# Performance work log

Measured on AMD Instinct MI355X. Metric: run time of the kernel, lower is better.

Reference implementation:

```python
import jax, jax.numpy as jnp
import numpy as np

N, E, F_NODE, F_EDGE, H, C = 25000, 50000, 7, 2, 4, 512
HC = H * C  # 2048


def setup_inputs() -> dict:
    key = jax.random.key(0)
    ks = jax.random.split(key, 20)
    p = lambda k, shp: (jax.random.normal(k, shp, dtype=jnp.float32) * 0.02)
    return {
        "x": jax.random.normal(ks[0], (N, F_NODE), dtype=jnp.float32),
        "edge_attr": jax.random.normal(ks[1], (E, F_EDGE), dtype=jnp.float32),
        "edge_index": jax.random.randint(ks[2], (2, E), 0, N, dtype=jnp.int64),
        "W_node": p(ks[3], (F_NODE, C)), "b_node": jnp.zeros((C,), jnp.float32),
        "W_edge": p(ks[4], (F_EDGE, C)), "b_edge": jnp.zeros((C,), jnp.float32),
        "W_l": p(ks[5], (C, HC)), "b_l": jnp.zeros((HC,), jnp.float32),
        "W_r": p(ks[6], (C, HC)), "b_r": jnp.zeros((HC,), jnp.float32),
        "W_le": p(ks[7], (C, HC)),  # lin_edge has no bias in PyG GATv2Conv
        "att": p(ks[8], (H, C)),
        "conv_bias": jnp.zeros((HC,), jnp.float32),
        "W_d1": p(ks[9], (HC, C)), "b_d1": jnp.zeros((C,), jnp.float32),
        "W_d2": p(ks[10], (C, 6)), "b_d2": jnp.zeros((6,), jnp.float32),
    }


def reference(x, edge_attr, edge_index, W_node, b_node, W_edge, b_edge,
              W_l, b_l, W_r, b_r, W_le, att, conv_bias, W_d1, b_d1, W_d2, b_d2):
    n = x.shape[0]
    src, dst = edge_index[0], edge_index[1]
    # encoders
    h = jax.nn.relu(x @ W_node + b_node)                  # [N, C]
    ea = jax.nn.relu(edge_attr @ W_edge + b_edge)         # [E, C]
    # GATv2Conv (heads=4, concat, edge_dim, add_self_loops=False)
    xl = (h @ W_l + b_l).reshape(n, H, C)                 # source transform
    xr = (h @ W_r + b_r).reshape(n, H, C)                 # target transform
    ee = (ea @ W_le).reshape(-1, H, C)                    # [E, H, C]
    m = xl[src] + xr[dst] + ee                            # [E, H, C]
    s = jax.nn.leaky_relu(m, negative_slope=0.2)
    logits = jnp.einsum('ehc,hc->eh', s, att)             # [E, H]
    # segment softmax over destination nodes
    mx = jax.ops.segment_max(logits, dst, num_segments=n)
    ex = jnp.exp(logits - mx[dst])
    den = jax.ops.segment_sum(ex, dst, num_segments=n)
    alpha = ex / (den[dst] + 1e-16)                       # [E, H]
    out = jax.ops.segment_sum(alpha[..., None] * xl[src], dst, num_segments=n)
    out = out.reshape(n, HC) + conv_bias                  # [N, 2048]
    # decoder + sigmoid (mode != 'train')
    pred = jax.nn.relu(out @ W_d1 + b_d1) @ W_d2 + b_d2   # [N, 6]
    return jax.nn.sigmoid(pred)
```

## Files before the change

kernel.cpp:

```cpp
#include <hip/hip_runtime.h>
#include <hip/hip_bf16.h>

typedef __attribute__((ext_vector_type(8))) short short8;
typedef __attribute__((ext_vector_type(4))) float f32x4;
typedef unsigned int uint32;

#define GLD16(g, l) __builtin_amdgcn_global_load_lds( \
    (const __attribute__((address_space(1))) unsigned int*)(g), \
    (__attribute__((address_space(3))) unsigned int*)(l), 16, 0, 0)

__device__ __forceinline__ float bfu(unsigned short u) {
    union { uint32 v; float f; } x; x.v = ((uint32)u) << 16; return x.f;
}
__device__ __forceinline__ void storev(float* p, float v) { *p = v; }
__device__ __forceinline__ void storev(__hip_bfloat16* p, float v) { *p = __float2bfloat16(v); }

__global__ __launch_bounds__(256) void transpose_bf16(
    const float* __restrict__ W, __hip_bfloat16* __restrict__ WT, int K, int N)
{
    __shared__ float tile[32][33];
    int k0 = blockIdx.x * 32, n0 = blockIdx.y * 32;
    int tx = threadIdx.x & 31, ty = threadIdx.x >> 5;
    #pragma unroll
    for (int i = 0; i < 32; i += 8)
        tile[ty + i][tx] = W[(size_t)(k0 + ty + i) * N + n0 + tx];
    __syncthreads();
    #pragma unroll
    for (int i = 0; i < 32; i += 8)
        WT[(size_t)(n0 + ty + i) * K + k0 + tx] = __float2bfloat16(tile[tx][ty + i]);
}

__global__ __launch_bounds__(256) void encode_nodes(
    const float* __restrict__ x, const float* __restrict__ Wn,
    const float* __restrict__ bn, __hip_bfloat16* __restrict__ h, int Nn)
{
    int idx = blockIdx.x * 256 + threadIdx.x;
    if (idx >= Nn * 512) return;
    int n = idx >> 9, c = idx & 511;
    float acc = bn[c];
    #pragma unroll
    for (int f = 0; f < 7; ++f) acc += x[n * 7 + f] * Wn[f * 512 + c];
    h[idx] = __float2bfloat16(fmaxf(acc, 0.f));
}

__global__ __launch_bounds__(256) void encode_edges(
    const float* __restrict__ eat, const float* __restrict__ We,
    const float* __restrict__ be, __hip_bfloat16* __restrict__ ea, int E)
{
    int idx = blockIdx.x * 256 + threadIdx.x;
    if (idx >= E * 512) return;
    int e = idx >> 9, c = idx & 511;
    float v = fmaf(eat[e * 2], We[c], fmaf(eat[e * 2 + 1], We[512 + c], be[c]));
    ea[idx] = __float2bfloat16(fmaxf(v, 0.f));
}

template <typename OutT, bool HAS_BIAS>
__global__ __launch_bounds__(256) void mfma_gemm(
    const __hip_bfloat16* __restrict__ A, int lda, long az,
    const __hip_bfloat16* __restrict__ BT, int ldb, long bz,
    const float* __restrict__ bias,
    OutT* __restrict__ C, int ldc, long cz, int M, int K)
{
    __shared__ uint4 As4[512];
    __shared__ uint4 Bs4[512];
    A  += (long)blockIdx.z * az;
    BT += (long)blockIdx.z * bz;
    C  += (long)blockIdx.z * cz;
    const int t = threadIdx.x, lane = t & 63, w = t >> 6;
    const int wr = (w >> 1) * 64, wc = (w & 1) * 64;
    const int col0 = blockIdx.x * 128, row0 = blockIdx.y * 128;
    const int lr = lane & 15, lg = lane >> 4;
    const int r0 = w * 16 + (lane >> 2);
    const int ksw = ((lane & 3) ^ ((lane >> 3) & 3)) * 8;
    const int rsw = (lg ^ ((lr >> 1) & 3)) << 4;

    const __hip_bfloat16* Ap0 = A + (size_t)(row0 + r0) * lda + ksw;
    const __hip_bfloat16* Ap1 = A + (size_t)(row0 + r0 + 64) * lda + ksw;
    const __hip_bfloat16* Bp0 = BT + (size_t)(col0 + r0) * ldb + ksw;
    const __hip_bfloat16* Bp1 = BT + (size_t)(col0 + r0 + 64) * ldb + ksw;
    char* AsB = (char*)As4; char* BsB = (char*)Bs4;
    uint4* la0 = As4 + w * 64;       uint4* la1 = As4 + (w + 4) * 64;
    uint4* lb0 = Bs4 + w * 64;       uint4* lb1 = Bs4 + (w + 4) * 64;

    f32x4 acc[4][4];
    #pragma unroll
    for (int m = 0; m < 4; ++m)
        #pragma unroll
        for (int n = 0; n < 4; ++n) acc[m][n] = 0.f;

    for (int k0 = 0; k0 < K; k0 += 32) {
        GLD16(Ap0 + k0, la0);
        GLD16(Ap1 + k0, la1);
        GLD16(Bp0 + k0, lb0);
        GLD16(Bp1 + k0, lb1);
        __syncthreads();
        short8 af[4], bfrag[4];
        #pragma unroll
        for (int m = 0; m < 4; ++m)
            af[m] = *(const short8*)(AsB + (wr + m * 16 + lr) * 64 + rsw);
        #pragma unroll
        for (int n = 0; n < 4; ++n)
            bfrag[n] = *(const short8*)(BsB + (wc + n * 16 + lr) * 64 + rsw);
        #pragma unroll
        for (int m = 0; m < 4; ++m)
            #pragma unroll
            for (int n = 0; n < 4; ++n)
                acc[m][n] = __builtin_amdgcn_mfma_f32_16x16x32_bf16(af[m], bfrag[n], acc[m][n], 0, 0, 0);
        __syncthreads();
    }

    #pragma unroll
    for (int m = 0; m < 4; ++m) {
        #pragma unroll
        for (int r = 0; r < 4; ++r) {
            int gr = row0 + wr + m * 16 + lg * 4 + r;
            if (gr >= M) continue;
            #pragma unroll
            for (int n = 0; n < 4; ++n) {
                int gc = col0 + wc + n * 16 + lr;
                float v = acc[m][n][r];
                if (HAS_BIAS) v += bias[gc];
                storev(&C[(size_t)gr * ldc + gc], v);
            }
        }
    }
}

__global__ __launch_bounds__(256) void edge_mfma_logits(
    const __hip_bfloat16* __restrict__ ea,
    const __hip_bfloat16* __restrict__ WleT,
    const __hip_bfloat16* __restrict__ XL,
    const __hip_bfloat16* __restrict__ XR,
    const int* __restrict__ ei,
    const float* __restrict__ att,
    float* __restrict__ logits,
    int E)
{
    __shared__ uint4 As4[512];
    __shared__ uint4 Bs4[512];
    __shared__ int srcs[128], dsts[128];
    const int t = threadIdx.x, lane = t & 63, w = t >> 6;
    const int wr = (w >> 1) * 64, wc = (w & 1) * 64;
    const int col0 = blockIdx.x * 128, row0 = blockIdx.y * 128;
    const int lr = lane & 15, lg = lane >> 4;
    const int r0 = w * 16 + (lane >> 2);
    const int ksw = ((lane & 3) ^ ((lane >> 3) & 3)) * 8;
    const int rsw = (lg ^ ((lr >> 1) & 3)) << 4;

    if (t < 128) {
        int ge = row0 + t;
        bool ok = ge < E;
        srcs[t] = ok ? ei[ge] : 0;
        dsts[t] = ok ? ei[E + ge] : 0;
    }
    char* AsB = (char*)As4; char* BsB = (char*)Bs4;
    uint4* la0 = As4 + w * 64;       uint4* la1 = As4 + (w + 4) * 64;
    uint4* lb0 = Bs4 + w * 64;       uint4* lb1 = Bs4 + (w + 4) * 64;
    const __hip_bfloat16* Ap0 = ea + (size_t)(row0 + r0) * 512 + ksw;
    const __hip_bfloat16* Ap1 = ea + (size_t)(row0 + r0 + 64) * 512 + ksw;
    const __hip_bfloat16* Bp0 = WleT + (size_t)(col0 + r0) * 512 + ksw;
    const __hip_bfloat16* Bp1 = WleT + (size_t)(col0 + r0 + 64) * 512 + ksw;
    __syncthreads();

    f32x4 acc[4][4];
    #pragma unroll
    for (int m = 0; m < 4; ++m)
        #pragma unroll
        for (int n = 0; n < 4; ++n) acc[m][n] = 0.f;

    for (int k0 = 0; k0 < 512; k0 += 32) {
        GLD16(Ap0 + k0, la0);
        GLD16(Ap1 + k0, la1);
        GLD16(Bp0 + k0, lb0);
        GLD16(Bp1 + k0, lb1);
        __syncthreads();
        short8 af[4], bfrag[4];
        #pragma unroll
        for (int m = 0; m < 4; ++m)
            af[m] = *(const short8*)(AsB + (wr + m * 16 + lr) * 64 + rsw);
        #pragma unroll
        for (int n = 0; n < 4; ++n)
            bfrag[n] = *(const short8*)(BsB + (wc + n * 16 + lr) * 64 + rsw);
        #pragma unroll
        for (int m = 0; m < 4; ++m)
            #pragma unroll
            for (int n = 0; n < 4; ++n)
                acc[m][n] = __builtin_amdgcn_mfma_f32_16x16x32_bf16(af[m], bfrag[n], acc[m][n], 0, 0, 0);
        __syncthreads();
    }

    const int hh = col0 >> 9;
    float attv[4];
    #pragma unroll
    for (int n = 0; n < 4; ++n)
        attv[n] = att[hh * 512 + ((col0 + wc + n * 16 + lr) & 511)];
    float part[4][4];
    #pragma unroll
    for (int m = 0; m < 4; ++m)
        #pragma unroll
        for (int r = 0; r < 4; ++r) part[m][r] = 0.f;

    const int prt = (lane & 3) * 8;
    #pragma unroll
    for (int ch = 0; ch < 4; ++ch) {
        __syncthreads();
        int cc = col0 + ch * 32;
        GLD16(XL + (size_t)srcs[r0] * 2048 + cc + prt, la0);
        GLD16(XL + (size_t)srcs[r0 + 64] * 2048 + cc + prt, la1);
        GLD16(XR + (size_t)dsts[r0] * 2048 + cc + prt, lb0);
        GLD16(XR + (size_t)dsts[r0 + 64] * 2048 + cc + prt, lb1);
        __syncthreads();
        #pragma unroll
        for (int n = 0; n < 4; ++n) {
            if (((wc + n * 16) >> 5) != ch) continue;
            int colin = ((n & 1) << 4) + lr;
            #pragma unroll
            for (int m = 0; m < 4; ++m) {
                #pragma unroll
                for (int r = 0; r < 4; ++r) {
                    int row = wr + m * 16 + lg * 4 + r;
                    float xl = bfu(*(const unsigned short*)(AsB + row * 64 + colin * 2));
                    float xr = bfu(*(const unsigned short*)(BsB + row * 64 + colin * 2));
                    float mv = acc[m][n][r] + xl + xr;
                    part[m][r] += attv[n] * ((mv > 0.f) ? mv : 0.2f * mv);
                }
            }
        }
    }
    #pragma unroll
    for (int m = 0; m < 4; ++m) {
        #pragma unroll
        for (int r = 0; r < 4; ++r) {
            float p = part[m][r];
            p += __shfl_xor(p, 1); p += __shfl_xor(p, 2);
            p += __shfl_xor(p, 4); p += __shfl_xor(p, 8);
            int ge = row0 + wr + m * 16 + lg * 4 + r;
            if (lr == 0 && ge < E) atomicAdd(&logits[ge * 4 + hh], p);
        }
    }
}

__global__ __launch_bounds__(256) void count_dst(
    const int* __restrict__ ei, int* __restrict__ cnt, int E)
{
    int e = blockIdx.x * 256 + threadIdx.x;
    if (e < E) atomicAdd(&cnt[ei[E + e]], 1);
}

__global__ __launch_bounds__(1024) void scan_kernel(
    const int* __restrict__ cnt, int* __restrict__ offs, int N)
{
    __shared__ int wsum[16];
    __shared__ int stot;
    __shared__ int carry_s;
    int t = threadIdx.x, lane = t & 63, w = t >> 6;
    if (t == 0) carry_s = 0;
    __syncthreads();
    for (int base = 0; base < N; base += 1024) {
        int v = (base + t < N) ? cnt[base + t] : 0;
        int x = v;
        #pragma unroll
        for (int off = 1; off < 64; off <<= 1) {
            int y = __shfl_up(x, off);
            if (lane >= off) x += y;
        }
        if (lane == 63) wsum[w] = x;
        __syncthreads();
        if (w == 0 && lane < 16) {
            int v0 = wsum[lane];
            int s = v0;
            #pragma unroll
            for (int off = 1; off < 16; off <<= 1) {
                int y = __shfl_up(s, off);
                if (lane >= off) s += y;
            }
            wsum[lane] = s - v0;
            if (lane == 15) stot = s;
        }
        __syncthreads();
        if (base + t < N) offs[base + t] = carry_s + wsum[w] + x - v;
        __syncthreads();
        if (t == 0) carry_s += stot;
    }
    __syncthreads();
    if (t == 0) offs[N] = carry_s;
}

__global__ __launch_bounds__(256) void fill_elist(
    const int* __restrict__ ei, const int* __restrict__ offs,
    int* __restrict__ cnt2, int* __restrict__ elist, int E)
{
    int e = blockIdx.x * 256 + threadIdx.x;
    if (e >= E) return;
    int d = ei[E + e];
    int p = offs[d] + atomicAdd(&cnt2[d], 1);
    elist[p] = e;
}

__global__ __launch_bounds__(256) void gat_out(
    const __hip_bfloat16* __restrict__ Y,
    const int* __restrict__ ei,
    const int* __restrict__ elist, const int* __restrict__ offs,
    const float* __restrict__ logits,
    const float* __restrict__ bias2,
    const float* __restrict__ Wd2,
    const float* __restrict__ bd2,
    float* __restrict__ out, int N, int E)
{
    __shared__ float wds[512 * 6];
    int t = threadIdx.x;
    for (int i = t; i < 512 * 6; i += 256) wds[i] = Wd2[i];
    __syncthreads();
    int w = t >> 6, lane = t & 63;
    int dst = blockIdx.x * 4 + w;
    if (dst >= N) return;
    int s = offs[dst], cntE = offs[dst + 1] - s;

    float den[4] = {0.f, 0.f, 0.f, 0.f};
    for (int i = 0; i < cntE; ++i) {
        int e = elist[s + i];
        #pragma unroll
        for (int h = 0; h < 4; ++h) den[h] += expf(logits[e * 4 + h]);
    }
    float acc[8] = {0.f, 0.f, 0.f, 0.f, 0.f, 0.f, 0.f, 0.f};
    for (int i = 0; i < cntE; ++i) {
        int e = elist[s + i];
        int src = ei[e];
        #pragma unroll
        for (int h = 0; h < 4; ++h) {
            float al = expf(logits[e * 4 + h]) / (den[h] + 1e-16f);
            uint4 q = *(const uint4*)((const unsigned short*)Y
                        + ((size_t)src * 4 + h) * 512 + lane * 8);
            acc[0] += al * bfu((unsigned short)(q.x & 0xffff));
            acc[1] += al * bfu((unsigned short)(q.x >> 16));
            acc[2] += al * bfu((unsigned short)(q.y & 0xffff));
            acc[3] += al * bfu((unsigned short)(q.y >> 16));
            acc[4] += al * bfu((unsigned short)(q.z & 0xffff));
            acc[5] += al * bfu((unsigned short)(q.z >> 16));
            acc[6] += al * bfu((unsigned short)(q.w & 0xffff));
            acc[7] += al * bfu((unsigned short)(q.w >> 16));
        }
    }
    float p[6] = {0.f, 0.f, 0.f, 0.f, 0.f, 0.f};
    #pragma unroll
    for (int j = 0; j < 8; ++j) {
        int c = lane * 8 + j;
        float u = fmaxf(acc[j] + bias2[c], 0.f);
        #pragma unroll
        for (int jj = 0; jj < 6; ++jj) p[jj] += u * wds[c * 6 + jj];
    }
    #pragma unroll
    for (int off = 32; off; off >>= 1)
        #pragma unroll
        for (int jj = 0; jj < 6; ++jj) p[jj] += __shfl_down(p[jj], off);
    if (lane == 0) {
        #pragma unroll
        for (int jj = 0; jj < 6; ++jj)
            out[(size_t)dst * 6 + jj] = 1.f / (1.f + expf(-(p[jj] + bd2[jj])));
    }
}

__global__ __launch_bounds__(256) void bias2_kernel(
    const float* __restrict__ bd1, const float* __restrict__ cb,
    const float* __restrict__ Wd1, float* __restrict__ bias2)
{
    int j = blockIdx.x * 256 + threadIdx.x;
    if (j >= 512) return;
    float acc = bd1[j];
    for (int k = 0; k < 2048; ++k) acc += cb[k] * Wd1[(size_t)k * 512 + j];
    bias2[j] = acc;
}

extern "C" void kernel_launch(void* const* d_in, const int* in_sizes, int n_in,
                              void* d_out, int out_size, void* d_ws, size_t ws_size,
                              hipStream_t stream)
{
    const float* x         = (const float*)d_in[0];
    const float* edge_attr = (const float*)d_in[1];
    const int*   ei        = (const int*)d_in[2];
    const float* W_node = (const float*)d_in[3],  *b_node = (const float*)d_in[4];
    const float* W_edge = (const float*)d_in[5],  *b_edge = (const float*)d_in[6];
    const float* W_l    = (const float*)d_in[7],  *b_l    = (const float*)d_in[8];
    const float* W_r    = (const float*)d_in[9],  *b_r    = (const float*)d_in[10];
    const float* W_le   = (const float*)d_in[11];
    const float* att    = (const float*)d_in[12];
    const float* conv_bias = (const float*)d_in[13];
    const float* W_d1   = (const float*)d_in[14], *b_d1 = (const float*)d_in[15];
    const float* W_d2   = (const float*)d_in[16], *b_d2 = (const float*)d_in[17];
    float* out = (float*)d_out;

    const int N = in_sizes[0] / 7;
    const int E = in_sizes[1] / 2;
    const int MP = (N + 127) & ~127;
    const int EP = (E + 127) & ~127;

    char* ws = (char*)d_ws;
    const size_t szR0 = (size_t)EP * 512 * 2;
    const size_t szX  = (size_t)MP * 2048 * 2;
    const size_t szW  = (size_t)2048 * 512 * 2;
    const size_t szlg = (size_t)E * 4 * 4;
    const size_t szI  = (((size_t)(N + 1) * 4) + 15) & ~(size_t)15;
    const size_t o_XL = szR0;
    const size_t o_XR = o_XL + szX;
    const size_t o_W  = o_XR + szX;
    const size_t o_lg = o_W + 4 * szW;
    const size_t o_b2 = o_lg + szlg;
    const size_t o_cnt = o_b2 + 2048;
    const size_t o_cnt2 = o_cnt + szI;
    const size_t o_off = o_cnt2 + szI;
    const size_t o_el = o_off + szI;
    const size_t need = o_el + (size_t)E * 4;
    if (ws_size < need) return;

    __hip_bfloat16* h   = (__hip_bfloat16*)ws;
    __hip_bfloat16* ea  = (__hip_bfloat16*)ws;
    __hip_bfloat16* XL  = (__hip_bfloat16*)(ws + o_XL);
    __hip_bfloat16* XR  = (__hip_bfloat16*)(ws + o_XR);
    __hip_bfloat16* Y   = XR;
    __hip_bfloat16* WlT = (__hip_bfloat16*)(ws + o_W);
    __hip_bfloat16* WrT = WlT + szW / 2;
    __hip_bfloat16* WleT= WrT + szW / 2;
    __hip_bfloat16* Wd1T= WleT + szW / 2;
    float* logits = (float*)(ws + o_lg);
    float* bias2  = (float*)(ws + o_b2);
    int* cnt   = (int*)(ws + o_cnt);
    int* cnt2  = (int*)(ws + o_cnt2);
    int* offs  = (int*)(ws + o_off);
    int* elist = (int*)(ws + o_el);

    hipMemsetAsync(logits, 0, szlg, stream);
    hipMemsetAsync(cnt, 0, szI, stream);
    hipMemsetAsync(cnt2, 0, szI, stream);

    dim3 gT(512 / 32, 2048 / 32);
    transpose_bf16<<<gT, 256, 0, stream>>>(W_l,  WlT, 512, 2048);
    transpose_bf16<<<gT, 256, 0, stream>>>(W_r,  WrT, 512, 2048);
    transpose_bf16<<<gT, 256, 0, stream>>>(W_le, WleT, 512, 2048);
    dim3 gT2(2048 / 32, 512 / 32);
    transpose_bf16<<<gT2, 256, 0, stream>>>(W_d1, Wd1T, 2048, 512);
    bias2_kernel<<<2, 256, 0, stream>>>(b_d1, conv_bias, W_d1, bias2);

    count_dst<<<(E + 255) / 256, 256, 0, stream>>>(ei, cnt, E);
    scan_kernel<<<1, 1024, 0, stream>>>(cnt, offs, N);
    fill_elist<<<(E + 255) / 256, 256, 0, stream>>>(ei, offs, cnt2, elist, E);

    encode_nodes<<<(N * 512 + 255) / 256, 256, 0, stream>>>(x, W_node, b_node, h, N);

    const int MB = MP / 128;
    dim3 gNode(2048 / 128, MB);
    mfma_gemm<__hip_bfloat16, true><<<gNode, 256, 0, stream>>>(
        h, 512, 0, WlT, 512, 0, b_l, XL, 2048, 0, N, 512);
    mfma_gemm<__hip_bfloat16, true><<<gNode, 256, 0, stream>>>(
        h, 512, 0, WrT, 512, 0, b_r, XR, 2048, 0, N, 512);

    encode_edges<<<(E * 512 + 255) / 256, 256, 0, stream>>>(edge_attr, W_edge, b_edge, ea, E);

    dim3 gE(16, EP / 128);
    edge_mfma_logits<<<gE, 256, 0, stream>>>(ea, WleT, XL, XR, ei, att, logits, E);

    dim3 gY(512 / 128, MB, 4);
    mfma_gemm<__hip_bfloat16, false><<<gY, 256, 0, stream>>>(
        XL, 2048, 512, Wd1T, 2048, 512, nullptr, Y, 2048, 512, N, 512);

    gat_out<<<(N + 3) / 4, 256, 0, stream>>>(Y, ei, elist, offs, logits,
                                             bias2, W_d2, b_d2, out, N, E);
}
```

Measured before the change: 784.8 us.

## Double-buffer LDS tiles with vmcnt-gated barriers in GEMM and edge-logit kernels

Turns the single-buffered K loop in the MFMA GEMM and the edge logits kernel into a double-buffered pipeline. The next tile's global-to-LDS loads are issued before computing on the current tile, and explicit s_waitcnt vmcnt barriers replace the two __syncthreads per iteration. The gathered XL/XR chunks in the epilogue are prefetched the same way, and the MFMA section runs at raised wave priority. This doubles LDS use per block, which may lower occupancy, and relies on hand-counted vmcnt values being correct.

```diff
diff --git a/kernel.cpp b/kernel.cpp
--- a/kernel.cpp
+++ b/kernel.cpp
@@ -8,6 +8,10 @@
 #define GLD16(g, l) __builtin_amdgcn_global_load_lds( \
     (const __attribute__((address_space(1))) unsigned int*)(g), \
     (__attribute__((address_space(3))) unsigned int*)(l), 16, 0, 0)
+
+#define BAR_VM4()  asm volatile("s_waitcnt vmcnt(4)\ns_barrier" ::: "memory")
+#define BAR_VM0()  asm volatile("s_waitcnt vmcnt(0)\ns_barrier" ::: "memory")
+#define BAR_LGKM() asm volatile("s_waitcnt lgkmcnt(0)\ns_barrier" ::: "memory")
 
 __device__ __forceinline__ float bfu(unsigned short u) {
     union { uint32 v; float f; } x; x.v = ((uint32)u) << 16; return x.f;
@@ -61,8 +65,8 @@
     const float* __restrict__ bias,
     OutT* __restrict__ C, int ldc, long cz, int M, int K)
 {
-    __shared__ uint4 As4[512];
-    __shared__ uint4 Bs4[512];
+    __shared__ uint4 As4[1024];
+    __shared__ uint4 Bs4[1024];
     A  += (long)blockIdx.z * az;
     BT += (long)blockIdx.z * bz;
     C  += (long)blockIdx.z * cz;
@@ -78,9 +82,6 @@
     const __hip_bfloat16* Ap1 = A + (size_t)(row0 + r0 + 64) * lda + ksw;
     const __hip_bfloat16* Bp0 = BT + (size_t)(col0 + r0) * ldb + ksw;
     const __hip_bfloat16* Bp1 = BT + (size_t)(col0 + r0 + 64) * ldb + ksw;
-    char* AsB = (char*)As4; char* BsB = (char*)Bs4;
-    uint4* la0 = As4 + w * 64;       uint4* la1 = As4 + (w + 4) * 64;
-    uint4* lb0 = Bs4 + w * 64;       uint4* lb1 = Bs4 + (w + 4) * 64;
 
     f32x4 acc[4][4];
     #pragma unroll
@@ -88,12 +89,27 @@
         #pragma unroll
         for (int n = 0; n < 4; ++n) acc[m][n] = 0.f;
 
-    for (int k0 = 0; k0 < K; k0 += 32) {
-        GLD16(Ap0 + k0, la0);
-        GLD16(Ap1 + k0, la1);
-        GLD16(Bp0 + k0, lb0);
-        GLD16(Bp1 + k0, lb1);
-        __syncthreads();
+    GLD16(Ap0, As4 + w * 64);
+    GLD16(Ap1, As4 + (w + 4) * 64);
+    GLD16(Bp0, Bs4 + w * 64);
+    GLD16(Bp1, Bs4 + (w + 4) * 64);
+
+    int cur = 0;
+    for (int k0 = 0; k0 < K; k0 += 32, cur ^= 1) {
+        int nk = k0 + 32;
+        if (nk < K) {
+            uint4* a = As4 + (cur ^ 1) * 512;
+            uint4* b = Bs4 + (cur ^ 1) * 512;
+            GLD16(Ap0 + nk, a + w * 64);
+            GLD16(Ap1 + nk, a + (w + 4) * 64);
+            GLD16(Bp0 + nk, b + w * 64);
+            GLD16(Bp1 + nk, b + (w + 4) * 64);
+            BAR_VM4();
+        } else {
+            BAR_VM0();
+        }
+        const char* AsB = (const char*)(As4 + cur * 512);
+        const char* BsB = (const char*)(Bs4 + cur * 512);
         short8 af[4], bfrag[4];
         #pragma unroll
         for (int m = 0; m < 4; ++m)
@@ -101,12 +117,14 @@
         #pragma unroll
         for (int n = 0; n < 4; ++n)
             bfrag[n] = *(const short8*)(BsB + (wc + n * 16 + lr) * 64 + rsw);
+        BAR_LGKM();
+        __builtin_amdgcn_s_setprio(1);
         #pragma unroll
         for (int m = 0; m < 4; ++m)
             #pragma unroll
             for (int n = 0; n < 4; ++n)
                 acc[m][n] = __builtin_amdgcn_mfma_f32_16x16x32_bf16(af[m], bfrag[n], acc[m][n], 0, 0, 0);
-        __syncthreads();
+        __builtin_amdgcn_s_setprio(0);
     }
 
     #pragma unroll
@@ -136,8 +154,8 @@
     float* __restrict__ logits,
     int E)
 {
-    __shared__ uint4 As4[512];
-    __shared__ uint4 Bs4[512];
+    __shared__ uint4 As4[1024];
+    __shared__ uint4 Bs4[1024];
     __shared__ int srcs[128], dsts[128];
     const int t = threadIdx.x, lane = t & 63, w = t >> 6;
     const int wr = (w >> 1) * 64, wc = (w & 1) * 64;
@@ -147,20 +165,23 @@
     const int ksw = ((lane & 3) ^ ((lane >> 3) & 3)) * 8;
     const int rsw = (lg ^ ((lr >> 1) & 3)) << 4;
 
+    const __hip_bfloat16* Ap0 = ea + (size_t)(row0 + r0) * 512 + ksw;
+    const __hip_bfloat16* Ap1 = ea + (size_t)(row0 + r0 + 64) * 512 + ksw;
+    const __hip_bfloat16* Bp0 = WleT + (size_t)(col0 + r0) * 512 + ksw;
+    const __hip_bfloat16* Bp1 = WleT + (size_t)(col0 + r0 + 64) * 512 + ksw;
+
+    GLD16(Ap0, As4 + w * 64);
+    GLD16(Ap1, As4 + (w + 4) * 64);
+    GLD16(Bp0, Bs4 + w * 64);
+    GLD16(Bp1, Bs4 + (w + 4) * 64);
+
     if (t < 128) {
         int ge = row0 + t;
         bool ok = ge < E;
         srcs[t] = ok ? ei[ge] : 0;
         dsts[t] = ok ? ei[E + ge] : 0;
     }
-    char* AsB = (char*)As4; char* BsB = (char*)Bs4;
-    uint4* la0 = As4 + w * 64;       uint4* la1 = As4 + (w + 4) * 64;
-    uint4* lb0 = Bs4 + w * 64;       uint4* lb1 = Bs4 + (w + 4) * 64;
-    const __hip_bfloat16* Ap0 = ea + (size_t)(row0 + r0) * 512 + ksw;
-    const __hip_bfloat16* Ap1 = ea + (size_t)(row0 + r0 + 64) * 512 + ksw;
-    const __hip_bfloat16* Bp0 = WleT + (size_t)(col0 + r0) * 512 + ksw;
-    const __hip_bfloat16* Bp1 = WleT + (size_t)(col0 + r0 + 64) * 512 + ksw;
-    __syncthreads();
+    BAR_LGKM();
 
     f32x4 acc[4][4];
     #pragma unroll
@@ -168,12 +189,22 @@
         #pragma unroll
         for (int n = 0; n < 4; ++n) acc[m][n] = 0.f;
 
-    for (int k0 = 0; k0 < 512; k0 += 32) {
-        GLD16(Ap0 + k0, la0);
-        GLD16(Ap1 + k0, la1);
-        GLD16(Bp0 + k0, lb0);
-        GLD16(Bp1 + k0, lb1);
-        __syncthreads();
+    int cur = 0;
+    for (int k0 = 0; k0 < 512; k0 += 32, cur ^= 1) {
+        int nk = k0 + 32;
+        if (nk < 512) {
+            uint4* a = As4 + (cur ^ 1) * 512;
+            uint4* b = Bs4 + (cur ^ 1) * 512;
+            GLD16(Ap0 + nk, a + w * 64);
+            GLD16(Ap1 + nk, a + (w + 4) * 64);
+            GLD16(Bp0 + nk, b + w * 64);
+            GLD16(Bp1 + nk, b + (w + 4) * 64);
+            BAR_VM4();
+        } else {
+            BAR_VM0();
+        }
+        const char* AsB = (const char*)(As4 + cur * 512);
+        const char* BsB = (const char*)(Bs4 + cur * 512);
         short8 af[4], bfrag[4];
         #pragma unroll
         for (int m = 0; m < 4; ++m)
@@ -181,12 +212,14 @@
         #pragma unroll
         for (int n = 0; n < 4; ++n)
             bfrag[n] = *(const short8*)(BsB + (wc + n * 16 + lr) * 64 + rsw);
+        BAR_LGKM();
+        __builtin_amdgcn_s_setprio(1);
         #pragma unroll
         for (int m = 0; m < 4; ++m)
             #pragma unroll
             for (int n = 0; n < 4; ++n)
                 acc[m][n] = __builtin_amdgcn_mfma_f32_16x16x32_bf16(af[m], bfrag[n], acc[m][n], 0, 0, 0);
-        __syncthreads();
+        __builtin_amdgcn_s_setprio(0);
     }
 
     const int hh = col0 >> 9;
@@ -201,15 +234,32 @@
         for (int r = 0; r < 4; ++r) part[m][r] = 0.f;
 
     const int prt = (lane & 3) * 8;
+    const int s0 = srcs[r0], s1 = srcs[r0 + 64];
+    const int d0 = dsts[r0], d1 = dsts[r0 + 64];
+
+    {
+        int cc = col0;
+        GLD16(XL + (size_t)s0 * 2048 + cc + prt, As4 + w * 64);
+        GLD16(XL + (size_t)s1 * 2048 + cc + prt, As4 + (w + 4) * 64);
+        GLD16(XR + (size_t)d0 * 2048 + cc + prt, Bs4 + w * 64);
+        GLD16(XR + (size_t)d1 * 2048 + cc + prt, Bs4 + (w + 4) * 64);
+    }
     #pragma unroll
     for (int ch = 0; ch < 4; ++ch) {
-        __syncthreads();
-        int cc = col0 + ch * 32;
-        GLD16(XL + (size_t)srcs[r0] * 2048 + cc + prt, la0);
-        GLD16(XL + (size_t)srcs[r0 + 64] * 2048 + cc + prt, la1);
-        GLD16(XR + (size_t)dsts[r0] * 2048 + cc + prt, lb0);
-        GLD16(XR + (size_t)dsts[r0 + 64] * 2048 + cc + prt, lb1);
-        __syncthreads();
+        if (ch < 3) {
+            uint4* a = As4 + ((ch + 1) & 1) * 512;
+            uint4* b = Bs4 + ((ch + 1) & 1) * 512;
+            int cc = col0 + (ch + 1) * 32;
+            GLD16(XL + (size_t)s0 * 2048 + cc + prt, a + w * 64);
+            GLD16(XL + (size_t)s1 * 2048 + cc + prt, a + (w + 4) * 64);
+            GLD16(XR + (size_t)d0 * 2048 + cc + prt, b + w * 64);
+            GLD16(XR + (size_t)d1 * 2048 + cc + prt, b + (w + 4) * 64);
+            BAR_VM4();
+        } else {
+            BAR_VM0();
+        }
+        const char* AsB = (const char*)(As4 + (ch & 1) * 512);
+        const char* BsB = (const char*)(Bs4 + (ch & 1) * 512);
         #pragma unroll
         for (int n = 0; n < 4; ++n) {
             if (((wc + n * 16) >> 5) != ch) continue;
@@ -226,6 +276,7 @@
                 }
             }
         }
+        BAR_LGKM();
     }
     #pragma unroll
     for (int m = 0; m < 4; ++m) {
```

Result: no change. 789.3 us (+0.6%).

## Process edges in destination-sorted order and batch XL/XR GEMMs into one launch

Applied to the files above, without the earlier changes.

Edges are permuted into CSR (destination-sorted) order before the edge encoder and logits kernel, so logits are written in sorted position and gat_out reads them contiguously without the elist indirection. Sorted src/dst arrays are written by fill_elist. The two node GEMMs (XL and XR) are merged into one launch via a z-dimension with a concatenated bias buffer, relying on XR directly following XL in the workspace. This trades an extra gather in encode_edges for better locality on XR[dst] gathers and in the aggregation.

```diff
diff --git a/kernel.cpp b/kernel.cpp
--- a/kernel.cpp
+++ b/kernel.cpp
@@ -43,13 +43,15 @@
     h[idx] = __float2bfloat16(fmaxf(acc, 0.f));
 }
 
-__global__ __launch_bounds__(256) void encode_edges(
-    const float* __restrict__ eat, const float* __restrict__ We,
-    const float* __restrict__ be, __hip_bfloat16* __restrict__ ea, int E)
+__global__ __launch_bounds__(256) void encode_edges_sorted(
+    const float* __restrict__ eat, const int* __restrict__ elist,
+    const float* __restrict__ We, const float* __restrict__ be,
+    __hip_bfloat16* __restrict__ ea, int E)
 {
     int idx = blockIdx.x * 256 + threadIdx.x;
     if (idx >= E * 512) return;
-    int e = idx >> 9, c = idx & 511;
+    int p = idx >> 9, c = idx & 511;
+    int e = elist[p];
     float v = fmaf(eat[e * 2], We[c], fmaf(eat[e * 2 + 1], We[512 + c], be[c]));
     ea[idx] = __float2bfloat16(fmaxf(v, 0.f));
 }
@@ -58,7 +60,7 @@
 __global__ __launch_bounds__(256) void mfma_gemm(
     const __hip_bfloat16* __restrict__ A, int lda, long az,
     const __hip_bfloat16* __restrict__ BT, int ldb, long bz,
-    const float* __restrict__ bias,
+    const float* __restrict__ bias, long biasz,
     OutT* __restrict__ C, int ldc, long cz, int M, int K)
 {
     __shared__ uint4 As4[512];
@@ -66,6 +68,7 @@
     A  += (long)blockIdx.z * az;
     BT += (long)blockIdx.z * bz;
     C  += (long)blockIdx.z * cz;
+    if (HAS_BIAS) bias += (long)blockIdx.z * biasz;
     const int t = threadIdx.x, lane = t & 63, w = t >> 6;
     const int wr = (w >> 1) * 64, wc = (w & 1) * 64;
     const int col0 = blockIdx.x * 128, row0 = blockIdx.y * 128;
@@ -131,7 +134,8 @@
     const __hip_bfloat16* __restrict__ WleT,
     const __hip_bfloat16* __restrict__ XL,
     const __hip_bfloat16* __restrict__ XR,
-    const int* __restrict__ ei,
+    const int* __restrict__ ssrc,
+    const int* __restrict__ sdst,
     const float* __restrict__ att,
     float* __restrict__ logits,
     int E)
@@ -150,8 +154,8 @@
     if (t < 128) {
         int ge = row0 + t;
         bool ok = ge < E;
-        srcs[t] = ok ? ei[ge] : 0;
-        dsts[t] = ok ? ei[E + ge] : 0;
+        srcs[t] = ok ? ssrc[ge] : 0;
+        dsts[t] = ok ? sdst[ge] : 0;
     }
     char* AsB = (char*)As4; char* BsB = (char*)Bs4;
     uint4* la0 = As4 + w * 64;       uint4* la1 = As4 + (w + 4) * 64;
@@ -288,24 +292,26 @@
 
 __global__ __launch_bounds__(256) void fill_elist(
     const int* __restrict__ ei, const int* __restrict__ offs,
-    int* __restrict__ cnt2, int* __restrict__ elist, int E)
+    int* __restrict__ cnt2, int* __restrict__ elist,
+    int* __restrict__ ssrc, int* __restrict__ sdst, int E)
 {
     int e = blockIdx.x * 256 + threadIdx.x;
     if (e >= E) return;
     int d = ei[E + e];
     int p = offs[d] + atomicAdd(&cnt2[d], 1);
     elist[p] = e;
+    ssrc[p] = ei[e];
+    sdst[p] = d;
 }
 
 __global__ __launch_bounds__(256) void gat_out(
     const __hip_bfloat16* __restrict__ Y,
-    const int* __restrict__ ei,
-    const int* __restrict__ elist, const int* __restrict__ offs,
+    const int* __restrict__ ssrc, const int* __restrict__ offs,
     const float* __restrict__ logits,
     const float* __restrict__ bias2,
     const float* __restrict__ Wd2,
     const float* __restrict__ bd2,
-    float* __restrict__ out, int N, int E)
+    float* __restrict__ out, int N)
 {
     __shared__ float wds[512 * 6];
     int t = threadIdx.x;
@@ -318,17 +324,16 @@
 
     float den[4] = {0.f, 0.f, 0.f, 0.f};
     for (int i = 0; i < cntE; ++i) {
-        int e = elist[s + i];
-        #pragma unroll
-        for (int h = 0; h < 4; ++h) den[h] += expf(logits[e * 4 + h]);
+        #pragma unroll
+        for (int h = 0; h < 4; ++h) den[h] += expf(logits[(s + i) * 4 + h]);
     }
     float acc[8] = {0.f, 0.f, 0.f, 0.f, 0.f, 0.f, 0.f, 0.f};
     for (int i = 0; i < cntE; ++i) {
-        int e = elist[s + i];
-        int src = ei[e];
+        int p = s + i;
+        int src = ssrc[p];
         #pragma unroll
         for (int h = 0; h < 4; ++h) {
-            float al = expf(logits[e * 4 + h]) / (den[h] + 1e-16f);
+            float al = expf(logits[p * 4 + h]) / (den[h] + 1e-16f);
             uint4 q = *(const uint4*)((const unsigned short*)Y
                         + ((size_t)src * 4 + h) * 512 + lane * 8);
             acc[0] += al * bfu((unsigned short)(q.x & 0xffff));
@@ -341,22 +346,22 @@
             acc[7] += al * bfu((unsigned short)(q.w >> 16));
         }
     }
-    float p[6] = {0.f, 0.f, 0.f, 0.f, 0.f, 0.f};
+    float p6[6] = {0.f, 0.f, 0.f, 0.f, 0.f, 0.f};
     #pragma unroll
     for (int j = 0; j < 8; ++j) {
         int c = lane * 8 + j;
         float u = fmaxf(acc[j] + bias2[c], 0.f);
         #pragma unroll
-        for (int jj = 0; jj < 6; ++jj) p[jj] += u * wds[c * 6 + jj];
+        for (int jj = 0; jj < 6; ++jj) p6[jj] += u * wds[c * 6 + jj];
     }
     #pragma unroll
     for (int off = 32; off; off >>= 1)
         #pragma unroll
-        for (int jj = 0; jj < 6; ++jj) p[jj] += __shfl_down(p[jj], off);
+        for (int jj = 0; jj < 6; ++jj) p6[jj] += __shfl_down(p6[jj], off);
     if (lane == 0) {
         #pragma unroll
         for (int jj = 0; jj < 6; ++jj)
-            out[(size_t)dst * 6 + jj] = 1.f / (1.f + expf(-(p[jj] + bd2[jj])));
+            out[(size_t)dst * 6 + jj] = 1.f / (1.f + expf(-(p6[jj] + bd2[jj])));
     }
 }
 
@@ -405,11 +410,14 @@
     const size_t o_W  = o_XR + szX;
     const size_t o_lg = o_W + 4 * szW;
     const size_t o_b2 = o_lg + szlg;
-    const size_t o_cnt = o_b2 + 2048;
+    const size_t o_bc = o_b2 + 2048;
+    const size_t o_cnt = o_bc + 4096 * 4;
     const size_t o_cnt2 = o_cnt + szI;
     const size_t o_off = o_cnt2 + szI;
     const size_t o_el = o_off + szI;
-    const size_t need = o_el + (size_t)E * 4;
+    const size_t o_ss = o_el + (size_t)E * 4;
+    const size_t o_sd = o_ss + (size_t)E * 4;
+    const size_t need = o_sd + (size_t)E * 4;
     if (ws_size < need) return;
 
     __hip_bfloat16* h   = (__hip_bfloat16*)ws;
@@ -423,14 +431,19 @@
     __hip_bfloat16* Wd1T= WleT + szW / 2;
     float* logits = (float*)(ws + o_lg);
     float* bias2  = (float*)(ws + o_b2);
+    float* bcat   = (float*)(ws + o_bc);
     int* cnt   = (int*)(ws + o_cnt);
     int* cnt2  = (int*)(ws + o_cnt2);
     int* offs  = (int*)(ws + o_off);
     int* elist = (int*)(ws + o_el);
+    int* ssrc  = (int*)(ws + o_ss);
+    int* sdst  = (int*)(ws + o_sd);
 
     hipMemsetAsync(logits, 0, szlg, stream);
     hipMemsetAsync(cnt, 0, szI, stream);
     hipMemsetAsync(cnt2, 0, szI, stream);
+    hipMemcpyAsync(bcat, b_l, 2048 * 4, hipMemcpyDeviceToDevice, stream);
+    hipMemcpyAsync(bcat + 2048, b_r, 2048 * 4, hipMemcpyDeviceToDevice, stream);
 
     dim3 gT(512 / 32, 2048 / 32);
     transpose_bf16<<<gT, 256, 0, stream>>>(W_l,  WlT, 512, 2048);
@@ -442,26 +455,26 @@
 
     count_dst<<<(E + 255) / 256, 256, 0, stream>>>(ei, cnt, E);
     scan_kernel<<<1, 1024, 0, stream>>>(cnt, offs, N);
-    fill_elist<<<(E + 255) / 256, 256, 0, stream>>>(ei, offs, cnt2, elist, E);
+    fill_elist<<<(E + 255) / 256, 256, 0, stream>>>(ei, offs, cnt2, elist, ssrc, sdst, E);
 
     encode_nodes<<<(N * 512 + 255) / 256, 256, 0, stream>>>(x, W_node, b_node, h, N);
 
     const int MB = MP / 128;
-    dim3 gNode(2048 / 128, MB);
+    dim3 gNode(2048 / 128, MB, 2);
     mfma_gemm<__hip_bfloat16, true><<<gNode, 256, 0, stream>>>(
-        h, 512, 0, WlT, 512, 0, b_l, XL, 2048, 0, N, 512);
-    mfma_gemm<__hip_bfloat16, true><<<gNode, 256, 0, stream>>>(
-        h, 512, 0, WrT, 512, 0, b_r, XR, 2048, 0, N, 512);
-
-    encode_edges<<<(E * 512 + 255) / 256, 256, 0, stream>>>(edge_attr, W_edge, b_edge, ea, E);
+        h, 512, 0, WlT, 512, (long)2048 * 512, bcat, 2048,
+        XL, 2048, (long)MP * 2048, N, 512);
+
+    encode_edges_sorted<<<(E * 512 + 255) / 256, 256, 0, stream>>>(
+        edge_attr, elist, W_edge, b_edge, ea, E);
 
     dim3 gE(16, EP / 128);
-    edge_mfma_logits<<<gE, 256, 0, stream>>>(ea, WleT, XL, XR, ei, att, logits, E);
+    edge_mfma_logits<<<gE, 256, 0, stream>>>(ea, WleT, XL, XR, ssrc, sdst, att, logits, E);
 
     dim3 gY(512 / 128, MB, 4);
     mfma_gemm<__hip_bfloat16, false><<<gY, 256, 0, stream>>>(
-        XL, 2048, 512, Wd1T, 2048, 512, nullptr, Y, 2048, 512, N, 512);
-
-    gat_out<<<(N + 3) / 4, 256, 0, stream>>>(Y, ei, elist, offs, logits,
-                                             bias2, W_d2, b_d2, out, N, E);
-}
+        XL, 2048, 512, Wd1T, 2048, 512, nullptr, 0, Y, 2048, 512, N, 512);
+
+    gat_out<<<(N + 3) / 4, 256, 0, stream>>>(Y, ssrc, offs, logits,
+                                             bias2, W_d2, b_d2, out, N);
+}
```

New measurement: 781.2 us. Within noise of the previous version (-0.5%).
